# Kernel tuning notes

Hardware: AMD Instinct MI355X
Metric: run time of the kernel (lower is better)

The kernel has to match this reference:

```python
import jax, jax.numpy as jnp
import numpy as np

N_NODES = 50000
N_EDGES = 800000
IN_CH, HID, HEADS, OUT_CH = 16, 64, 4, 8
NEG_SLOPE = 0.2


def _add_self_loops(edge_index, num_nodes):
    loop = jnp.arange(num_nodes, dtype=edge_index.dtype)
    loops = jnp.stack([loop, loop])  # [2, N]
    return jnp.concatenate([edge_index, loops], axis=1)


def _gat_conv(x, src, dst, W, a_src, a_dst, bias, concat):
    """PyG-style GATConv: linear -> per-edge LeakyReLU attention -> segment
    softmax over incoming edges -> scatter-add aggregate."""
    N = x.shape[0]
    H, C = a_src.shape
    h = (x @ W).reshape(N, H, C)                      # [N,H,C]
    alpha_src = (h * a_src).sum(-1)                   # [N,H]
    alpha_dst = (h * a_dst).sum(-1)                   # [N,H]
    e = jax.nn.leaky_relu(alpha_src[src] + alpha_dst[dst], NEG_SLOPE)  # [E,H]
    # numerically stable segment softmax over edges grouped by dst
    e_max = jax.ops.segment_max(e, dst, num_segments=N)
    e_exp = jnp.exp(e - e_max[dst])
    denom = jax.ops.segment_sum(e_exp, dst, num_segments=N)
    alpha = e_exp / denom[dst]                        # [E,H]
    msg = h[src] * alpha[:, :, None]                  # [E,H,C]
    out = jax.ops.segment_sum(msg, dst, num_segments=N)  # [N,H,C]
    if concat:
        return out.reshape(N, H * C) + bias
    return out.mean(axis=1) + bias


def setup_inputs() -> dict:
    key = jax.random.key(0)
    ks = jax.random.split(key, 12)
    s = 0.1
    return {
        "x": jax.random.normal(ks[0], (N_NODES, IN_CH), jnp.float32),
        "edge_index": jax.random.randint(ks[1], (2, N_EDGES), 0, N_NODES, jnp.int64),
        "W1": jax.random.normal(ks[2], (IN_CH, HEADS * HID), jnp.float32) * s,
        "as1": jax.random.normal(ks[3], (HEADS, HID), jnp.float32) * s,
        "ad1": jax.random.normal(ks[4], (HEADS, HID), jnp.float32) * s,
        "b1": jnp.zeros((HEADS * HID,), jnp.float32),
        "W2": jax.random.normal(ks[5], (HEADS * HID, HEADS * HID), jnp.float32) * s,
        "as2": jax.random.normal(ks[6], (HEADS, HID), jnp.float32) * s,
        "ad2": jax.random.normal(ks[7], (HEADS, HID), jnp.float32) * s,
        "b2": jnp.zeros((HID,), jnp.float32),
        "Wc": jax.random.normal(ks[8], (HID, OUT_CH), jnp.float32) * s,
        "bc": jnp.zeros((OUT_CH,), jnp.float32),
    }


def reference(x, edge_index, W1, as1, ad1, b1, W2, as2, ad2, b2, Wc, bc):
    ei = _add_self_loops(edge_index, x.shape[0])
    src, dst = ei[0], ei[1]
    h = _gat_conv(x, src, dst, W1, as1, ad1, b1, concat=True)
    h = jax.nn.elu(h)
    h = _gat_conv(h, src, dst, W2, as2, ad2, b2, concat=False)
    h = jax.nn.elu(h)
    return h @ Wc + bc  # [N, OUT_CH]
```

## Files before the change

### kernel.cpp

```cpp
#include <hip/hip_runtime.h>
#include <math.h>

#define NODES   50000
#define HEADS   4
#define HID     64
#define FDIM    256
#define IN_CH   16
#define NEG_SLOPE 0.2f

typedef unsigned short ushort_t;
typedef unsigned int uint_t;
typedef __attribute__((ext_vector_type(8))) short bf16x8;
typedef __attribute__((ext_vector_type(4))) float f32x4;
typedef __attribute__((ext_vector_type(2))) float f32x2;

__device__ inline ushort_t f2bf(float f) {
    uint_t u = __float_as_uint(f);
    u += 0x7fffu + ((u >> 16) & 1u);
    return (ushort_t)(u >> 16);
}
__device__ inline void unpack2(uint_t u, float& a, float& b) {
    a = __uint_as_float(u << 16);
    b = __uint_as_float(u & 0xffff0000u);
}


__global__ void k_hist(const int* __restrict__ ei, int E, int N, int* __restrict__ deg) {
    int e = blockIdx.x * blockDim.x + threadIdx.x;
    int Etot = E + N;
    if (e >= Etot) return;
    int d = (e < E) ? ei[E + e] : (e - E);
    if (d >= 0 && d < N) atomicAdd(&deg[d], 1);
}


__global__ __launch_bounds__(256) void k_scanA(const int* __restrict__ deg,
                                               int* __restrict__ bsum, int N) {
    __shared__ int sh[256];
    int t = threadIdx.x;
    int i0 = blockIdx.x * 4096 + t * 16;
    int s = 0;
#pragma unroll
    for (int j = 0; j < 16; ++j) s += (i0 + j < N) ? deg[i0 + j] : 0;
    sh[t] = s;
    __syncthreads();
    for (int off = 128; off; off >>= 1) {
        if (t < off) sh[t] += sh[t + off];
        __syncthreads();
    }
    if (t == 0) bsum[blockIdx.x] = sh[0];
}

__global__ void k_scanB(int* __restrict__ bsum, int* __restrict__ rowst, int nb, int N) {
    int t = threadIdx.x;
    int orig = (t < nb) ? bsum[t] : 0;
    int v = orig;
#pragma unroll
    for (int off = 1; off < 64; off <<= 1) {
        int u = __shfl_up(v, off);
        if (t >= off) v += u;
    }
    if (t < nb) bsum[t] = v - orig;
    if (t == 63) rowst[N] = v;
}

__global__ __launch_bounds__(256) void k_scanC(const int* __restrict__ deg,
                                               const int* __restrict__ bsum,
                                               int* __restrict__ rowst,
                                               int* __restrict__ cursor, int N) {
    __shared__ int sh[256];
    int t = threadIdx.x, b = blockIdx.x;
    int i0 = b * 4096 + t * 16;
    int v[16], s = 0;
#pragma unroll
    for (int j = 0; j < 16; ++j) { v[j] = (i0 + j < N) ? deg[i0 + j] : 0; s += v[j]; }
    sh[t] = s;
    __syncthreads();
    for (int off = 1; off < 256; off <<= 1) {
        int u = (t >= off) ? sh[t - off] : 0;
        __syncthreads();
        sh[t] += u;
        __syncthreads();
    }
    int excl = sh[t] - s + bsum[b];
#pragma unroll
    for (int j = 0; j < 16; ++j) {
        if (i0 + j < N) { rowst[i0 + j] = excl; cursor[i0 + j] = excl; }
        excl += v[j];
    }
}

__global__ void k_scatter(const int* __restrict__ ei, int E, int N,
                          int* __restrict__ cursor, int* __restrict__ csr_src,
                          int* __restrict__ csr_dst) {
    int e = blockIdx.x * blockDim.x + threadIdx.x;
    int Etot = E + N;
    if (e >= Etot) return;
    int s, d;
    if (e < E) { s = ei[e]; d = ei[E + e]; } else { s = d = e - E; }
    if (d < 0 || d >= N) return;
    int pos = atomicAdd(&cursor[d], 1);
    csr_src[pos] = s;
    csr_dst[pos] = d;
}


__global__ void k_prep(const float* __restrict__ x, const float* __restrict__ W1,
                       const float* __restrict__ W2, ushort_t* __restrict__ h,
                       ushort_t* __restrict__ W2T, int Nn) {
    int bid = blockIdx.x, tid = threadIdx.x;
    if (bid < 256) {
        int idx = bid * 256 + tid;
        int n = idx >> 8, k = idx & 255;
        W2T[idx] = f2bf(W2[k * FDIM + n]);
    } else {
        int idx = (bid - 256) * 256 + tid;
        if (idx >= Nn * FDIM) return;
        int n = idx >> 8, c = idx & 255;
        const float* xp = x + n * IN_CH;
        float s = 0.f;
#pragma unroll
        for (int k = 0; k < IN_CH; ++k) s += xp[k] * W1[k * FDIM + c];
        h[idx] = f2bf(s);
    }
}


__global__ __launch_bounds__(256) void k_gemm2(const ushort_t* __restrict__ A,
                                               const ushort_t* __restrict__ BT,
                                               ushort_t* __restrict__ C, int M) {
    __shared__ short As[64 * 40];
    __shared__ short Bs[64 * 40];
    int tid = threadIdx.x;
    int row0 = blockIdx.y * 64, col0 = blockIdx.x * 64;
    int wid = tid >> 6, lane = tid & 63;
    int wm = wid >> 1, wn = wid & 1;
    int quad = lane >> 4, lm = lane & 15;
    int lr = tid >> 2, lk = (tid & 3) * 8;
    f32x4 acc[2][2] = {};
    for (int k0 = 0; k0 < FDIM; k0 += 32) {
        uint4 av = {0u, 0u, 0u, 0u};
        int ar = row0 + lr;
        if (ar < M) av = *(const uint4*)(A + (long)ar * FDIM + k0 + lk);
        *(uint4*)(&As[lr * 40 + lk]) = av;
        uint4 bv = *(const uint4*)(BT + (long)(col0 + lr) * FDIM + k0 + lk);
        *(uint4*)(&Bs[lr * 40 + lk]) = bv;
        __syncthreads();
        bf16x8 a0 = *(const bf16x8*)(&As[(wm * 32 + lm) * 40 + quad * 8]);
        bf16x8 a1 = *(const bf16x8*)(&As[(wm * 32 + 16 + lm) * 40 + quad * 8]);
        bf16x8 b0 = *(const bf16x8*)(&Bs[(wn * 32 + lm) * 40 + quad * 8]);
        bf16x8 b1 = *(const bf16x8*)(&Bs[(wn * 32 + 16 + lm) * 40 + quad * 8]);
        acc[0][0] = __builtin_amdgcn_mfma_f32_16x16x32_bf16(a0, b0, acc[0][0], 0, 0, 0);
        acc[0][1] = __builtin_amdgcn_mfma_f32_16x16x32_bf16(a0, b1, acc[0][1], 0, 0, 0);
        acc[1][0] = __builtin_amdgcn_mfma_f32_16x16x32_bf16(a1, b0, acc[1][0], 0, 0, 0);
        acc[1][1] = __builtin_amdgcn_mfma_f32_16x16x32_bf16(a1, b1, acc[1][1], 0, 0, 0);
        __syncthreads();
    }
#pragma unroll
    for (int mi = 0; mi < 2; ++mi)
#pragma unroll
        for (int ni = 0; ni < 2; ++ni)
#pragma unroll
            for (int r = 0; r < 4; ++r) {
                int row = row0 + wm * 32 + mi * 16 + quad * 4 + r;
                int col = col0 + wn * 32 + ni * 16 + lm;
                if (row < M) C[(long)row * FDIM + col] = f2bf(acc[mi][ni][r]);
            }
}


__global__ void k_alpha(const ushort_t* __restrict__ h, const float* __restrict__ a_s,
                        const float* __restrict__ a_d, float* __restrict__ asrc,
                        float* __restrict__ adst, int Nn) {
    int idx = blockIdx.x * blockDim.x + threadIdx.x;
    if (idx >= Nn * HEADS) return;
    int n = idx >> 2, hh = idx & 3;
    const uint4* hp = (const uint4*)(h + (long)n * FDIM + hh * HID);
    const float* asp = a_s + hh * HID;
    const float* adp = a_d + hh * HID;
    float s1 = 0.f, s2 = 0.f;
#pragma unroll
    for (int q = 0; q < 8; ++q) {
        uint4 u = hp[q];
        float f[8];
        unpack2(u.x, f[0], f[1]); unpack2(u.y, f[2], f[3]);
        unpack2(u.z, f[4], f[5]); unpack2(u.w, f[6], f[7]);
#pragma unroll
        for (int j = 0; j < 8; ++j) { s1 += f[j] * asp[q * 8 + j]; s2 += f[j] * adp[q * 8 + j]; }
    }
    asrc[idx] = s1;
    adst[idx] = s2;
}


__global__ void k_pw(const int* __restrict__ csr_src, const int* __restrict__ csr_dst,
                     const float* __restrict__ asrc, const float* __restrict__ adst,
                     int2* __restrict__ pwb, int Etot) {
    int e = blockIdx.x * blockDim.x + threadIdx.x;
    if (e >= Etot) return;
    int s = csr_src[e], d = csr_dst[e];
    float4 av = *(const float4*)(asrc + s * 4);
    float4 dv = *(const float4*)(adst + d * 4);
    float t[4] = {av.x + dv.x, av.y + dv.y, av.z + dv.z, av.w + dv.w};
    int soff = s << 9;
#pragma unroll
    for (int h = 0; h < 4; ++h) {
        float tt = (t[h] > 0.f) ? t[h] : NEG_SLOPE * t[h];
        pwb[h * Etot + e] = make_int2(soff, __float_as_int(__expf(tt)));
    }
}


__device__ inline void fma8(f32x2& a0, f32x2& a1, f32x2& a2, f32x2& a3,
                            uint4 hv, float pw) {
    f32x2 p = {pw, pw};
    f32x2 u;
    u.x = __uint_as_float(hv.x << 16); u.y = __uint_as_float(hv.x & 0xffff0000u);
    a0 += p * u;
    u.x = __uint_as_float(hv.y << 16); u.y = __uint_as_float(hv.y & 0xffff0000u);
    a1 += p * u;
    u.x = __uint_as_float(hv.z << 16); u.y = __uint_as_float(hv.z & 0xffff0000u);
    a2 += p * u;
    u.x = __uint_as_float(hv.w << 16); u.y = __uint_as_float(hv.w & 0xffff0000u);
    a3 += p * u;
}

__global__ __launch_bounds__(256) void k_agg(const ushort_t* __restrict__ h,
                                             const int2* __restrict__ pwb,
                                             const int* __restrict__ row_start,
                                             const float* __restrict__ bias,
                                             ushort_t* __restrict__ outp, int mode,
                                             int Etot, int N) {
    int tid  = threadIdx.x;
    int hh   = tid >> 6;
    int lane = tid & 63;
    int half = lane >> 5;
    int l32  = lane & 31;
    int g    = l32 >> 3;
    int cg   = l32 & 7;
    int d    = blockIdx.x * 2 + half;
    bool valid = d < N;
    int s0 = 0, s1 = 0;
    if (valid) { s0 = row_start[d]; s1 = row_start[d + 1]; }
    int cnt  = s1 - s0;
    int maxc = max(cnt, __shfl_xor(cnt, 32));
    const int2* pwp = pwb + (long)hh * Etot;
    int hoff = (hh * HID + cg * 8) * 2;

    f32x2 a0 = {0.f, 0.f}, a1 = {0.f, 0.f}, a2 = {0.f, 0.f}, a3 = {0.f, 0.f};
    float den = 0.f;

    for (int off = 0; off < maxc; off += 8) {
        int idx0 = s0 + off + g;
        int idx1 = idx0 + 4;
        int2 ep0 = (idx0 < s1) ? pwp[idx0] : make_int2(0, 0);
        int2 ep1 = (idx1 < s1) ? pwp[idx1] : make_int2(0, 0);
        uint4 hv0 = *(const uint4*)((const char*)h + (uint_t)ep0.x + hoff);
        uint4 hv1 = *(const uint4*)((const char*)h + (uint_t)ep1.x + hoff);
        float pw0 = __int_as_float(ep0.y), pw1 = __int_as_float(ep1.y);
        den += pw0 + pw1;
        fma8(a0, a1, a2, a3, hv0, pw0);
        fma8(a0, a1, a2, a3, hv1, pw1);
    }
#pragma unroll
    for (int off = 8; off <= 16; off <<= 1) {
        a0.x += __shfl_xor(a0.x, off); a0.y += __shfl_xor(a0.y, off);
        a1.x += __shfl_xor(a1.x, off); a1.y += __shfl_xor(a1.y, off);
        a2.x += __shfl_xor(a2.x, off); a2.y += __shfl_xor(a2.y, off);
        a3.x += __shfl_xor(a3.x, off); a3.y += __shfl_xor(a3.y, off);
        den  += __shfl_xor(den, off);
    }
    if (g == 0 && valid) {
        float inv = 1.f / den;
        float v[8] = {a0.x, a0.y, a1.x, a1.y, a2.x, a2.y, a3.x, a3.y};
#pragma unroll
        for (int j = 0; j < 8; ++j) v[j] *= inv;
        if (mode) {
            const float* bp = bias + hh * HID + cg * 8;
#pragma unroll
            for (int j = 0; j < 8; ++j) {
                float t = v[j] + bp[j];
                v[j] = (t > 0.f) ? t : __expf(t) - 1.f;
            }
        }
        uint4 u;
        u.x = (uint_t)f2bf(v[0]) | ((uint_t)f2bf(v[1]) << 16);
        u.y = (uint_t)f2bf(v[2]) | ((uint_t)f2bf(v[3]) << 16);
        u.z = (uint_t)f2bf(v[4]) | ((uint_t)f2bf(v[5]) << 16);
        u.w = (uint_t)f2bf(v[6]) | ((uint_t)f2bf(v[7]) << 16);
        *(uint4*)(outp + (long)d * FDIM + hh * HID + cg * 8) = u;
    }
}


__global__ __launch_bounds__(256) void k_meanout(const ushort_t* __restrict__ agg,
                                                 const float* __restrict__ b2p,
                                                 const float* __restrict__ Wc,
                                                 const float* __restrict__ bc,
                                                 float* __restrict__ out, int N) {
    __shared__ float z[64][65];
    __shared__ float w[HID * 8 + 8];
    int tid = threadIdx.x;
    int n0 = blockIdx.x * 64;
    for (int i = tid; i < HID * 8; i += 256) w[i] = Wc[i];
    if (tid < 8) w[HID * 8 + tid] = bc[tid];
#pragma unroll
    for (int i = 0; i < 8; ++i) {
        int idx = i * 256 + tid;
        int n = idx >> 5, cp = idx & 31;
        int row = n0 + n;
        float va = 0.f, vb = 0.f;
        if (row < N) {
            const uint_t* p = (const uint_t*)(agg + (long)row * FDIM);
            uint_t u0 = p[cp], u1 = p[32 + cp], u2 = p[64 + cp], u3 = p[96 + cp];
            float x0, y0, x1, y1, x2, y2, x3, y3;
            unpack2(u0, x0, y0); unpack2(u1, x1, y1);
            unpack2(u2, x2, y2); unpack2(u3, x3, y3);
            va = 0.25f * (x0 + x1 + x2 + x3) + b2p[cp * 2];
            vb = 0.25f * (y0 + y1 + y2 + y3) + b2p[cp * 2 + 1];
            va = (va > 0.f) ? va : __expf(va) - 1.f;
            vb = (vb > 0.f) ? vb : __expf(vb) - 1.f;
        }
        z[n][cp * 2] = va;
        z[n][cp * 2 + 1] = vb;
    }
    __syncthreads();
#pragma unroll
    for (int i = 0; i < 2; ++i) {
        int idx = i * 256 + tid;
        int n = idx >> 3, o = idx & 7;
        int row = n0 + n;
        if (row < N) {
            float acc = w[HID * 8 + o];
#pragma unroll 8
            for (int c = 0; c < HID; ++c) acc += z[n][c] * w[c * 8 + o];
            out[(long)row * 8 + o] = acc;
        }
    }
}


extern "C" void kernel_launch(void* const* d_in, const int* in_sizes, int n_in,
                              void* d_out, int out_size, void* d_ws, size_t ws_size,
                              hipStream_t stream) {
    const float* x   = (const float*)d_in[0];
    const int*   ei  = (const int*)d_in[1];
    const float* W1  = (const float*)d_in[2];
    const float* as1 = (const float*)d_in[3];
    const float* ad1 = (const float*)d_in[4];
    const float* b1  = (const float*)d_in[5];
    const float* W2  = (const float*)d_in[6];
    const float* as2 = (const float*)d_in[7];
    const float* ad2 = (const float*)d_in[8];
    const float* b2  = (const float*)d_in[9];
    const float* Wc  = (const float*)d_in[10];
    const float* bc  = (const float*)d_in[11];
    float* out = (float*)d_out;

    const int N = NODES;
    const int E = in_sizes[1] / 2;
    const int Etot = E + N;

    char* ws = (char*)d_ws;
    size_t off = 0;
    auto alloc = [&](size_t bytes) {
        void* p = ws + off;
        off = (off + bytes + 255) & ~(size_t)255;
        return p;
    };
    ushort_t* hbf    = (ushort_t*)alloc((size_t)N * FDIM * 2);
    ushort_t* bufAct = (ushort_t*)alloc((size_t)N * FDIM * 2);
    float*    asrc   = (float*)alloc((size_t)N * HEADS * 4);
    float*    adst   = (float*)alloc((size_t)N * HEADS * 4);
    ushort_t* W2T    = (ushort_t*)alloc((size_t)FDIM * FDIM * 2);
    int*      deg    = (int*)alloc((size_t)N * 4);
    int*      rowst  = (int*)alloc((size_t)(N + 1) * 4);
    int*      cursor = (int*)alloc((size_t)N * 4);
    int*      bsum   = (int*)alloc(64 * 4);
    int*      csr    = (int*)alloc((size_t)Etot * 4);
    int*      csrd   = (int*)alloc((size_t)Etot * 4);
    int2*     pwb    = (int2*)alloc((size_t)Etot * HEADS * 8);

    const int tpb = 256;
    int egrid = (Etot + tpb - 1) / tpb;
    int nb = (N + 4095) / 4096;

    hipMemsetAsync(deg, 0, (size_t)N * 4, stream);
    k_hist<<<egrid, tpb, 0, stream>>>(ei, E, N, deg);
    k_scanA<<<nb, 256, 0, stream>>>(deg, bsum, N);
    k_scanB<<<1, 64, 0, stream>>>(bsum, rowst, nb, N);
    k_scanC<<<nb, 256, 0, stream>>>(deg, bsum, rowst, cursor, N);
    k_scatter<<<egrid, tpb, 0, stream>>>(ei, E, N, cursor, csr, csrd);

    k_prep<<<256 + (N * FDIM + tpb - 1) / tpb, tpb, 0, stream>>>(x, W1, W2, hbf, W2T, N);
    k_alpha<<<(N * HEADS + tpb - 1) / tpb, tpb, 0, stream>>>(hbf, as1, ad1, asrc, adst, N);
    k_pw<<<egrid, tpb, 0, stream>>>(csr, csrd, asrc, adst, pwb, Etot);
    k_agg<<<(N + 1) / 2, 256, 0, stream>>>(hbf, pwb, rowst, b1, bufAct, 1, Etot, N);

    dim3 g2(FDIM / 64, (N + 63) / 64);
    k_gemm2<<<g2, 256, 0, stream>>>(bufAct, W2T, hbf, N);
    k_alpha<<<(N * HEADS + tpb - 1) / tpb, tpb, 0, stream>>>(hbf, as2, ad2, asrc, adst, N);
    k_pw<<<egrid, tpb, 0, stream>>>(csr, csrd, asrc, adst, pwb, Etot);
    k_agg<<<(N + 1) / 2, 256, 0, stream>>>(hbf, pwb, rowst, nullptr, bufAct, 0, Etot, N);

    k_meanout<<<(N + 63) / 64, 256, 0, stream>>>(bufAct, b2, Wc, bc, out, N);
}
```

Before: 463.1 us.

## Fuse layer-1 attention logits into prep, pack edge weights, fuse final head into aggregation

The layer-1 prep kernel now computes one node per block and reduces the attention logits with wave shuffles, which removes the separate k_alpha pass for layer 1. Per-edge weights shrink from 8-byte int2 to a 4-byte word (16-bit source index plus an fp16 exp value), and the CSR src/dst arrays become one int2 array. The aggregation loop is unrolled to 16 edges per iteration, and the layer-2 head mean, ELU and final linear are fused into the aggregation epilogue, so k_meanout and its intermediate buffer go away. The packing assumes fewer than 65536 nodes, and the fp16 weights lose precision and range. The fused epilogue also adds block barriers and leaves most threads idle during the small output matmul.

```diff
diff --git a/kernel.cpp b/kernel.cpp
--- a/kernel.cpp
+++ b/kernel.cpp
@@ -23,6 +23,15 @@
     a = __uint_as_float(u << 16);
     b = __uint_as_float(u & 0xffff0000u);
 }
+__device__ inline uint_t f2h(float f) {
+    _Float16 h = (_Float16)f;
+    return (uint_t)*(ushort_t*)&h;
+}
+__device__ inline float h2f(uint_t u) {
+    ushort_t us = (ushort_t)u;
+    _Float16 h = *(_Float16*)&us;
+    return (float)h;
+}
 
 
 __global__ void k_hist(const int* __restrict__ ei, int E, int N, int* __restrict__ deg) {
@@ -32,7 +41,6 @@
     int d = (e < E) ? ei[E + e] : (e - E);
     if (d >= 0 && d < N) atomicAdd(&deg[d], 1);
 }
-
 
 __global__ __launch_bounds__(256) void k_scanA(const int* __restrict__ deg,
                                                int* __restrict__ bsum, int N) {
@@ -91,8 +99,7 @@
 }
 
 __global__ void k_scatter(const int* __restrict__ ei, int E, int N,
-                          int* __restrict__ cursor, int* __restrict__ csr_src,
-                          int* __restrict__ csr_dst) {
+                          int* __restrict__ cursor, int2* __restrict__ csr2) {
     int e = blockIdx.x * blockDim.x + threadIdx.x;
     int Etot = E + N;
     if (e >= Etot) return;
@@ -100,28 +107,48 @@
     if (e < E) { s = ei[e]; d = ei[E + e]; } else { s = d = e - E; }
     if (d < 0 || d >= N) return;
     int pos = atomicAdd(&cursor[d], 1);
-    csr_src[pos] = s;
-    csr_dst[pos] = d;
-}
-
-
-__global__ void k_prep(const float* __restrict__ x, const float* __restrict__ W1,
-                       const float* __restrict__ W2, ushort_t* __restrict__ h,
-                       ushort_t* __restrict__ W2T, int Nn) {
-    int bid = blockIdx.x, tid = threadIdx.x;
-    if (bid < 256) {
-        int idx = bid * 256 + tid;
+    csr2[pos] = make_int2(s, d);
+}
+
+
+__global__ __launch_bounds__(256) void k_prep1(const float* __restrict__ x,
+                                               const float* __restrict__ W1,
+                                               const float* __restrict__ as1,
+                                               const float* __restrict__ ad1,
+                                               const float* __restrict__ W2,
+                                               ushort_t* __restrict__ h,
+                                               float* __restrict__ asrc,
+                                               float* __restrict__ adst,
+                                               ushort_t* __restrict__ W2T, int Nn) {
+    int bid = blockIdx.x, t = threadIdx.x;
+    if (bid >= Nn) {
+        int idx = (bid - Nn) * 256 + t;
         int n = idx >> 8, k = idx & 255;
         W2T[idx] = f2bf(W2[k * FDIM + n]);
-    } else {
-        int idx = (bid - 256) * 256 + tid;
-        if (idx >= Nn * FDIM) return;
-        int n = idx >> 8, c = idx & 255;
-        const float* xp = x + n * IN_CH;
-        float s = 0.f;
-#pragma unroll
-        for (int k = 0; k < IN_CH; ++k) s += xp[k] * W1[k * FDIM + c];
-        h[idx] = f2bf(s);
+        return;
+    }
+    const float4* xp = (const float4*)(x + bid * IN_CH);
+    float4 x0 = xp[0], x1 = xp[1], x2 = xp[2], x3 = xp[3];
+    float s = x0.x * W1[t]            + x0.y * W1[FDIM + t]
+            + x0.z * W1[2 * FDIM + t] + x0.w * W1[3 * FDIM + t]
+            + x1.x * W1[4 * FDIM + t] + x1.y * W1[5 * FDIM + t]
+            + x1.z * W1[6 * FDIM + t] + x1.w * W1[7 * FDIM + t]
+            + x2.x * W1[8 * FDIM + t] + x2.y * W1[9 * FDIM + t]
+            + x2.z * W1[10 * FDIM + t]+ x2.w * W1[11 * FDIM + t]
+            + x3.x * W1[12 * FDIM + t]+ x3.y * W1[13 * FDIM + t]
+            + x3.z * W1[14 * FDIM + t]+ x3.w * W1[15 * FDIM + t];
+    h[(long)bid * FDIM + t] = f2bf(s);
+    float p1 = s * as1[t];
+    float p2 = s * ad1[t];
+#pragma unroll
+    for (int off = 1; off < 64; off <<= 1) {
+        p1 += __shfl_xor(p1, off);
+        p2 += __shfl_xor(p2, off);
+    }
+    if ((t & 63) == 0) {
+        int hh = t >> 6;
+        asrc[bid * 4 + hh] = p1;
+        adst[bid * 4 + hh] = p2;
     }
 }
 
@@ -193,20 +220,19 @@
 }
 
 
-__global__ void k_pw(const int* __restrict__ csr_src, const int* __restrict__ csr_dst,
-                     const float* __restrict__ asrc, const float* __restrict__ adst,
-                     int2* __restrict__ pwb, int Etot) {
+__global__ void k_pw(const int2* __restrict__ csr2, const float* __restrict__ asrc,
+                     const float* __restrict__ adst, uint_t* __restrict__ pwb, int Etot) {
     int e = blockIdx.x * blockDim.x + threadIdx.x;
     if (e >= Etot) return;
-    int s = csr_src[e], d = csr_dst[e];
-    float4 av = *(const float4*)(asrc + s * 4);
-    float4 dv = *(const float4*)(adst + d * 4);
+    int2 sd = csr2[e];
+    float4 av = *(const float4*)(asrc + sd.x * 4);
+    float4 dv = *(const float4*)(adst + sd.y * 4);
     float t[4] = {av.x + dv.x, av.y + dv.y, av.z + dv.z, av.w + dv.w};
-    int soff = s << 9;
+    uint_t sh = (uint_t)sd.x << 16;
 #pragma unroll
     for (int h = 0; h < 4; ++h) {
         float tt = (t[h] > 0.f) ? t[h] : NEG_SLOPE * t[h];
-        pwb[h * Etot + e] = make_int2(soff, __float_as_int(__expf(tt)));
+        pwb[h * Etot + e] = sh | f2h(__expf(tt));
     }
 }
 
@@ -226,11 +252,17 @@
 }
 
 __global__ __launch_bounds__(256) void k_agg(const ushort_t* __restrict__ h,
-                                             const int2* __restrict__ pwb,
+                                             const uint_t* __restrict__ pwb,
                                              const int* __restrict__ row_start,
-                                             const float* __restrict__ bias,
-                                             ushort_t* __restrict__ outp, int mode,
-                                             int Etot, int N) {
+                                             const float* __restrict__ b1,
+                                             const float* __restrict__ b2,
+                                             const float* __restrict__ Wc,
+                                             const float* __restrict__ bc,
+                                             ushort_t* __restrict__ hout,
+                                             float* __restrict__ fout,
+                                             int mode, int Etot, int N) {
+    __shared__ float zsh[2 * FDIM];
+    __shared__ float wsh[584];
     int tid  = threadIdx.x;
     int hh   = tid >> 6;
     int lane = tid & 63;
@@ -240,27 +272,39 @@
     int cg   = l32 & 7;
     int d    = blockIdx.x * 2 + half;
     bool valid = d < N;
+
+    if (!mode) {
+        for (int i = tid; i < 584; i += 256)
+            wsh[i] = (i < 512) ? Wc[i] : ((i < 520) ? bc[i - 512] : b2[i - 520]);
+    }
+
     int s0 = 0, s1 = 0;
     if (valid) { s0 = row_start[d]; s1 = row_start[d + 1]; }
     int cnt  = s1 - s0;
     int maxc = max(cnt, __shfl_xor(cnt, 32));
-    const int2* pwp = pwb + (long)hh * Etot;
-    int hoff = (hh * HID + cg * 8) * 2;
+    const uint_t* pwp = pwb + (long)hh * Etot;
+    const char* hbase = (const char*)h + (hh * HID + cg * 8) * 2;
 
     f32x2 a0 = {0.f, 0.f}, a1 = {0.f, 0.f}, a2 = {0.f, 0.f}, a3 = {0.f, 0.f};
     float den = 0.f;
 
-    for (int off = 0; off < maxc; off += 8) {
-        int idx0 = s0 + off + g;
-        int idx1 = idx0 + 4;
-        int2 ep0 = (idx0 < s1) ? pwp[idx0] : make_int2(0, 0);
-        int2 ep1 = (idx1 < s1) ? pwp[idx1] : make_int2(0, 0);
-        uint4 hv0 = *(const uint4*)((const char*)h + (uint_t)ep0.x + hoff);
-        uint4 hv1 = *(const uint4*)((const char*)h + (uint_t)ep1.x + hoff);
-        float pw0 = __int_as_float(ep0.y), pw1 = __int_as_float(ep1.y);
-        den += pw0 + pw1;
+    for (int off = 0; off < maxc; off += 16) {
+        int i0 = s0 + off + g;
+        uint_t u0 = (i0      < s1) ? pwp[i0]      : 0u;
+        uint_t u1 = (i0 + 4  < s1) ? pwp[i0 + 4]  : 0u;
+        uint_t u2 = (i0 + 8  < s1) ? pwp[i0 + 8]  : 0u;
+        uint_t u3 = (i0 + 12 < s1) ? pwp[i0 + 12] : 0u;
+        uint4 hv0 = *(const uint4*)(hbase + ((size_t)(u0 >> 16) << 9));
+        uint4 hv1 = *(const uint4*)(hbase + ((size_t)(u1 >> 16) << 9));
+        uint4 hv2 = *(const uint4*)(hbase + ((size_t)(u2 >> 16) << 9));
+        uint4 hv3 = *(const uint4*)(hbase + ((size_t)(u3 >> 16) << 9));
+        float pw0 = h2f(u0 & 0xffffu), pw1 = h2f(u1 & 0xffffu);
+        float pw2 = h2f(u2 & 0xffffu), pw3 = h2f(u3 & 0xffffu);
+        den += (pw0 + pw1) + (pw2 + pw3);
         fma8(a0, a1, a2, a3, hv0, pw0);
         fma8(a0, a1, a2, a3, hv1, pw1);
+        fma8(a0, a1, a2, a3, hv2, pw2);
+        fma8(a0, a1, a2, a3, hv3, pw3);
     }
 #pragma unroll
     for (int off = 8; off <= 16; off <<= 1) {
@@ -270,71 +314,55 @@
         a3.x += __shfl_xor(a3.x, off); a3.y += __shfl_xor(a3.y, off);
         den  += __shfl_xor(den, off);
     }
-    if (g == 0 && valid) {
-        float inv = 1.f / den;
-        float v[8] = {a0.x, a0.y, a1.x, a1.y, a2.x, a2.y, a3.x, a3.y};
-#pragma unroll
-        for (int j = 0; j < 8; ++j) v[j] *= inv;
-        if (mode) {
-            const float* bp = bias + hh * HID + cg * 8;
+
+    if (mode) {
+        if (g == 0 && valid) {
+            float inv = 1.f / den;
+            float v[8] = {a0.x, a0.y, a1.x, a1.y, a2.x, a2.y, a3.x, a3.y};
+            const float* bp = b1 + hh * HID + cg * 8;
 #pragma unroll
             for (int j = 0; j < 8; ++j) {
-                float t = v[j] + bp[j];
+                float t = v[j] * inv + bp[j];
                 v[j] = (t > 0.f) ? t : __expf(t) - 1.f;
             }
+            uint4 u;
+            u.x = (uint_t)f2bf(v[0]) | ((uint_t)f2bf(v[1]) << 16);
+            u.y = (uint_t)f2bf(v[2]) | ((uint_t)f2bf(v[3]) << 16);
+            u.z = (uint_t)f2bf(v[4]) | ((uint_t)f2bf(v[5]) << 16);
+            u.w = (uint_t)f2bf(v[6]) | ((uint_t)f2bf(v[7]) << 16);
+            *(uint4*)(hout + (long)d * FDIM + hh * HID + cg * 8) = u;
         }
-        uint4 u;
-        u.x = (uint_t)f2bf(v[0]) | ((uint_t)f2bf(v[1]) << 16);
-        u.y = (uint_t)f2bf(v[2]) | ((uint_t)f2bf(v[3]) << 16);
-        u.z = (uint_t)f2bf(v[4]) | ((uint_t)f2bf(v[5]) << 16);
-        u.w = (uint_t)f2bf(v[6]) | ((uint_t)f2bf(v[7]) << 16);
-        *(uint4*)(outp + (long)d * FDIM + hh * HID + cg * 8) = u;
-    }
-}
-
-
-__global__ __launch_bounds__(256) void k_meanout(const ushort_t* __restrict__ agg,
-                                                 const float* __restrict__ b2p,
-                                                 const float* __restrict__ Wc,
-                                                 const float* __restrict__ bc,
-                                                 float* __restrict__ out, int N) {
-    __shared__ float z[64][65];
-    __shared__ float w[HID * 8 + 8];
-    int tid = threadIdx.x;
-    int n0 = blockIdx.x * 64;
-    for (int i = tid; i < HID * 8; i += 256) w[i] = Wc[i];
-    if (tid < 8) w[HID * 8 + tid] = bc[tid];
-#pragma unroll
-    for (int i = 0; i < 8; ++i) {
-        int idx = i * 256 + tid;
-        int n = idx >> 5, cp = idx & 31;
-        int row = n0 + n;
-        float va = 0.f, vb = 0.f;
-        if (row < N) {
-            const uint_t* p = (const uint_t*)(agg + (long)row * FDIM);
-            uint_t u0 = p[cp], u1 = p[32 + cp], u2 = p[64 + cp], u3 = p[96 + cp];
-            float x0, y0, x1, y1, x2, y2, x3, y3;
-            unpack2(u0, x0, y0); unpack2(u1, x1, y1);
-            unpack2(u2, x2, y2); unpack2(u3, x3, y3);
-            va = 0.25f * (x0 + x1 + x2 + x3) + b2p[cp * 2];
-            vb = 0.25f * (y0 + y1 + y2 + y3) + b2p[cp * 2 + 1];
-            va = (va > 0.f) ? va : __expf(va) - 1.f;
-            vb = (vb > 0.f) ? vb : __expf(vb) - 1.f;
+    } else {
+        if (g == 0 && valid) {
+            float inv = 1.f / den;
+            float v[8] = {a0.x, a0.y, a1.x, a1.y, a2.x, a2.y, a3.x, a3.y};
+            int zb = half * FDIM + hh * HID + cg * 8;
+#pragma unroll
+            for (int j = 0; j < 8; ++j) zsh[zb + j] = v[j] * inv;
         }
-        z[n][cp * 2] = va;
-        z[n][cp * 2 + 1] = vb;
-    }
-    __syncthreads();
-#pragma unroll
-    for (int i = 0; i < 2; ++i) {
-        int idx = i * 256 + tid;
-        int n = idx >> 3, o = idx & 7;
-        int row = n0 + n;
-        if (row < N) {
-            float acc = w[HID * 8 + o];
+        __syncthreads();
+        if (tid < 128) {
+            int node = tid >> 6, c = tid & 63;
+            int dd = blockIdx.x * 2 + node;
+            if (dd < N) {
+                const float* zp = zsh + node * FDIM;
+                float zv = 0.25f * (zp[c] + zp[64 + c] + zp[128 + c] + zp[192 + c])
+                         + wsh[520 + c];
+                zv = (zv > 0.f) ? zv : __expf(zv) - 1.f;
+                zsh[node * FDIM + c] = zv;
+            }
+        }
+        __syncthreads();
+        if (tid < 16) {
+            int node = tid >> 3, o = tid & 7;
+            int dd = blockIdx.x * 2 + node;
+            if (dd < N) {
+                float acc = wsh[512 + o];
+                const float* zp = zsh + node * FDIM;
 #pragma unroll 8
-            for (int c = 0; c < HID; ++c) acc += z[n][c] * w[c * 8 + o];
-            out[(long)row * 8 + o] = acc;
+                for (int c = 0; c < 64; ++c) acc += zp[c] * wsh[c * 8 + o];
+                fout[(long)dd * 8 + o] = acc;
+            }
         }
     }
 }
@@ -369,7 +397,7 @@
         return p;
     };
     ushort_t* hbf    = (ushort_t*)alloc((size_t)N * FDIM * 2);
-    ushort_t* bufAct = (ushort_t*)alloc((size_t)N * FDIM * 2);
+    ushort_t* hact   = (ushort_t*)alloc((size_t)N * FDIM * 2);
     float*    asrc   = (float*)alloc((size_t)N * HEADS * 4);
     float*    adst   = (float*)alloc((size_t)N * HEADS * 4);
     ushort_t* W2T    = (ushort_t*)alloc((size_t)FDIM * FDIM * 2);
@@ -377,9 +405,8 @@
     int*      rowst  = (int*)alloc((size_t)(N + 1) * 4);
     int*      cursor = (int*)alloc((size_t)N * 4);
     int*      bsum   = (int*)alloc(64 * 4);
-    int*      csr    = (int*)alloc((size_t)Etot * 4);
-    int*      csrd   = (int*)alloc((size_t)Etot * 4);
-    int2*     pwb    = (int2*)alloc((size_t)Etot * HEADS * 8);
+    int2*     csr2   = (int2*)alloc((size_t)Etot * 8);
+    uint_t*   pwb    = (uint_t*)alloc((size_t)Etot * HEADS * 4);
 
     const int tpb = 256;
     int egrid = (Etot + tpb - 1) / tpb;
@@ -390,18 +417,17 @@
     k_scanA<<<nb, 256, 0, stream>>>(deg, bsum, N);
     k_scanB<<<1, 64, 0, stream>>>(bsum, rowst, nb, N);
     k_scanC<<<nb, 256, 0, stream>>>(deg, bsum, rowst, cursor, N);
-    k_scatter<<<egrid, tpb, 0, stream>>>(ei, E, N, cursor, csr, csrd);
-
-    k_prep<<<256 + (N * FDIM + tpb - 1) / tpb, tpb, 0, stream>>>(x, W1, W2, hbf, W2T, N);
-    k_alpha<<<(N * HEADS + tpb - 1) / tpb, tpb, 0, stream>>>(hbf, as1, ad1, asrc, adst, N);
-    k_pw<<<egrid, tpb, 0, stream>>>(csr, csrd, asrc, adst, pwb, Etot);
-    k_agg<<<(N + 1) / 2, 256, 0, stream>>>(hbf, pwb, rowst, b1, bufAct, 1, Etot, N);
+    k_scatter<<<egrid, tpb, 0, stream>>>(ei, E, N, cursor, csr2);
+
+    k_prep1<<<N + 256, 256, 0, stream>>>(x, W1, as1, ad1, W2, hbf, asrc, adst, W2T, N);
+    k_pw<<<egrid, tpb, 0, stream>>>(csr2, asrc, adst, pwb, Etot);
+    k_agg<<<(N + 1) / 2, 256, 0, stream>>>(hbf, pwb, rowst, b1, nullptr, nullptr, nullptr,
+                                           hact, nullptr, 1, Etot, N);
 
     dim3 g2(FDIM / 64, (N + 63) / 64);
-    k_gemm2<<<g2, 256, 0, stream>>>(bufAct, W2T, hbf, N);
+    k_gemm2<<<g2, 256, 0, stream>>>(hact, W2T, hbf, N);
     k_alpha<<<(N * HEADS + tpb - 1) / tpb, tpb, 0, stream>>>(hbf, as2, ad2, asrc, adst, N);
-    k_pw<<<egrid, tpb, 0, stream>>>(csr, csrd, asrc, adst, pwb, Etot);
-    k_agg<<<(N + 1) / 2, 256, 0, stream>>>(hbf, pwb, rowst, nullptr, bufAct, 0, Etot, N);
-
-    k_meanout<<<(N + 63) / 64, 256, 0, stream>>>(bufAct, b2, Wc, bc, out, N);
-}
+    k_pw<<<egrid, tpb, 0, stream>>>(csr2, asrc, adst, pwb, Etot);
+    k_agg<<<(N + 1) / 2, 256, 0, stream>>>(hbf, pwb, rowst, nullptr, b2, Wc, bc,
+                                           nullptr, out, 0, Etot, N);
+}
```

Result: faster. 403.2 us (-12.9%).
